# Kernel optimization log

Measured on AMD Instinct MI355X. Metric: run time of the kernel, lower is better.

The kernel has to match this reference:

```python
import jax, jax.numpy as jnp
import numpy as np

N, E, F_IN, HID, HEADS, NGRAPH = 50000, 800000, 256, 128, 4, 50
NEG_SLOPE = 0.2


def gat_conv(x, src, dst, W, a_src, a_dst, bias, heads, ch, concat):
    # x: [N, F_in]; W: [F_in, heads*ch]; a_src/a_dst: [heads, ch]; bias: [heads*ch] or [ch]
    n = x.shape[0]
    h = (x @ W).reshape(n, heads, ch)                      # [N,H,C]
    alpha_s = (h * a_src).sum(-1)                          # [N,H]
    alpha_d = (h * a_dst).sum(-1)                          # [N,H]
    e = jax.nn.leaky_relu(alpha_s[src] + alpha_d[dst], NEG_SLOPE)  # [E,H]
    # segment softmax over incoming edges of each destination node
    emax = jax.ops.segment_max(e, dst, num_segments=n)
    ex = jnp.exp(e - emax[dst])
    denom = jax.ops.segment_sum(ex, dst, num_segments=n)
    alpha = ex / (denom[dst] + 1e-16)                      # [E,H]
    msg = h[src] * alpha[:, :, None]                       # [E,H,C]
    out = jax.ops.segment_sum(msg, dst, num_segments=n)    # [N,H,C]
    out = out.reshape(n, heads * ch) if concat else out.mean(axis=1)
    return out + bias


def setup_inputs() -> dict:
    key = jax.random.key(0)
    ks = jax.random.split(key, 16)
    x = jax.random.normal(ks[0], (N, F_IN), dtype=jnp.float32)
    edge_index = jax.random.randint(ks[1], (2, E), 0, N, dtype=jnp.int64)
    batch = jnp.sort(jax.random.randint(ks[2], (N,), 0, NGRAPH, dtype=jnp.int64))
    s = 0.05
    return {
        "x": x, "edge_index": edge_index, "batch": batch,
        "W1": jax.random.normal(ks[3], (F_IN, HEADS * HID)) * s,
        "a1s": jax.random.normal(ks[4], (HEADS, HID)) * s,
        "a1d": jax.random.normal(ks[5], (HEADS, HID)) * s,
        "b1": jnp.zeros((HEADS * HID,), jnp.float32),
        "W2": jax.random.normal(ks[6], (HEADS * HID, HEADS * HID)) * s,
        "a2s": jax.random.normal(ks[7], (HEADS, HID)) * s,
        "a2d": jax.random.normal(ks[8], (HEADS, HID)) * s,
        "b2": jnp.zeros((HEADS * HID,), jnp.float32),
        "W3": jax.random.normal(ks[9], (HEADS * HID, HID)) * s,
        "a3s": jax.random.normal(ks[10], (1, HID)) * s,
        "a3d": jax.random.normal(ks[11], (1, HID)) * s,
        "b3": jnp.zeros((HID,), jnp.float32),
    }


def reference(x, edge_index, batch, W1, a1s, a1d, b1, W2, a2s, a2d, b2, W3, a3s, a3d, b3):
    src, dst = edge_index[0], edge_index[1]
    h = gat_conv(x, src, dst, W1, a1s, a1d, b1, HEADS, HID, True)
    h = jax.nn.elu(h)
    h = gat_conv(h, src, dst, W2, a2s, a2d, b2, HEADS, HID, True)
    h = jax.nn.elu(h)
    node_emb = gat_conv(h, src, dst, W3, a3s, a3d, b3, 1, HID, False)
    # global mean pool per graph
    sums = jax.ops.segment_sum(node_emb, batch, num_segments=NGRAPH)
    counts = jax.ops.segment_sum(jnp.ones((node_emb.shape[0],), node_emb.dtype), batch, num_segments=NGRAPH)
    graph_emb = sums / jnp.maximum(counts, 1.0)[:, None]
    return node_emb, graph_emb
```

## Files before the change

kernel.cpp:

```cpp
#include <hip/hip_runtime.h>
#include <hip/hip_bf16.h>

#define NN 50000
#define EE 800000
#define FIN 256
#define HIDC 128
#define NGRAPH 50
#define POOL_CHUNKS 32

typedef __attribute__((ext_vector_type(8))) short bf16x8;
typedef __attribute__((ext_vector_type(4))) float f32x4;

__device__ __forceinline__ float lrelu(float x) { return x > 0.f ? x : 0.2f * x; }

__device__ __forceinline__ unsigned short f2bf(float f) {
  union { float f; unsigned u; } c; c.f = f;
  unsigned u = c.u;
  unsigned r = (u + 0x7fffu + ((u >> 16) & 1u)) >> 16;
  return (unsigned short)r;
}
__device__ __forceinline__ float bf2f(unsigned short b) {
  union { unsigned u; float f; } c; c.u = ((unsigned)b) << 16;
  return c.f;
}

__global__ void hist_kernel(const int* __restrict__ dst, int* __restrict__ deg) {
  int e = blockIdx.x * blockDim.x + threadIdx.x;
  if (e < EE) atomicAdd(&deg[dst[e]], 1);
}

__global__ __launch_bounds__(1024)
void scan_kernel(const int* __restrict__ deg, int* __restrict__ indptr,
                 int* __restrict__ cursor) {
  __shared__ int wsum[16];
  const int tid = threadIdx.x;
  const int lane = tid & 63, wid = tid >> 6;
  const int PER = (NN + 1023) / 1024;
  int base = tid * PER;
  int n = NN - base; if (n < 0) n = 0; if (n > PER) n = PER;
  int sum = 0;
  for (int j = 0; j < n; j++) sum += deg[base + j];
  int inc = sum;
#pragma unroll
  for (int off = 1; off < 64; off <<= 1) {
    int t = __shfl_up(inc, off);
    if (lane >= off) inc += t;
  }
  if (lane == 63) wsum[wid] = inc;
  __syncthreads();
  if (tid == 0) {
    int run = 0;
#pragma unroll
    for (int w = 0; w < 16; w++) { int t = wsum[w]; wsum[w] = run; run += t; }
  }
  __syncthreads();
  int excl = wsum[wid] + inc - sum;
  int running = excl;
  for (int j = 0; j < n; j++) {
    int d = deg[base + j];
    indptr[base + j] = running;
    cursor[base + j] = running;
    running += d;
  }
  if (tid == 1023) indptr[NN] = excl + sum;
}

__global__ void scatter_kernel(const int* __restrict__ src, const int* __restrict__ dst,
                               int* __restrict__ cursor, int* __restrict__ csr_src) {
  int e = blockIdx.x * blockDim.x + threadIdx.x;
  if (e < EE) {
    int d = dst[e];
    int slot = atomicAdd(&cursor[d], 1);
    csr_src[slot] = src[e];
  }
}

__global__ __launch_bounds__(256)
void transpose_split(const float* __restrict__ W, unsigned short* __restrict__ WtHi,
                     unsigned short* __restrict__ WtLo, int K, int N) {
  __shared__ float t[32][33];
  int k0 = blockIdx.y * 32, n0 = blockIdx.x * 32;
  int tx = threadIdx.x & 31, ty = threadIdx.x >> 5;
  for (int r = ty; r < 32; r += 8) t[r][tx] = W[(size_t)(k0 + r) * N + n0 + tx];
  __syncthreads();
  for (int r = ty; r < 32; r += 8) {
    float v = t[tx][r];
    unsigned short hb = f2bf(v);
    size_t o = (size_t)(n0 + r) * K + k0 + tx;
    WtHi[o] = hb;
    WtLo[o] = f2bf(v - bf2f(hb));
  }
}

__global__ void split_x(const float* __restrict__ in, unsigned short* __restrict__ hi,
                        unsigned short* __restrict__ lo, int n4) {
  int i = blockIdx.x * blockDim.x + threadIdx.x;
  if (i >= n4) return;
  float4 v = ((const float4*)in)[i];
  unsigned short h[4], l[4];
  float a[4] = {v.x, v.y, v.z, v.w};
#pragma unroll
  for (int j = 0; j < 4; j++) { h[j] = f2bf(a[j]); l[j] = f2bf(a[j] - bf2f(h[j])); }
  ((ushort4*)hi)[i] = make_ushort4(h[0], h[1], h[2], h[3]);
  ((ushort4*)lo)[i] = make_ushort4(l[0], l[1], l[2], l[3]);
}

__global__ __launch_bounds__(256)
void gemm_split(const unsigned short* __restrict__ Ahi, const unsigned short* __restrict__ Alo,
                const unsigned short* __restrict__ Bhi, const unsigned short* __restrict__ Blo,
                float* __restrict__ C, int M, int K, int Ncols) {
  __shared__ unsigned short smem[4 * 128 * 32];
  const int tid = threadIdx.x;
  const int lane = tid & 63;
  const int wid = tid >> 6;
  const int wr = wid >> 1, wc = wid & 1;
  const int brow0 = blockIdx.y * 128, bcol0 = blockIdx.x * 128;

  f32x4 acc[4][4];
#pragma unroll
  for (int i = 0; i < 4; i++)
#pragma unroll
    for (int j = 0; j < 4; j++) acc[i][j] = (f32x4){0.f, 0.f, 0.f, 0.f};

  for (int k0 = 0; k0 < K; k0 += 32) {
#pragma unroll
    for (int t = 0; t < 8; t++) {
      const int tile = t >> 1;
      const int s = ((t & 1) << 8) + tid;
      const int row = s >> 2;
      const int cl = (s & 3) ^ ((row >> 1) & 3);
      const unsigned short* gsrc;
      if (tile < 2) {
        int grow = brow0 + row; if (grow > M - 1) grow = M - 1;
        const unsigned short* base = (tile == 0) ? Ahi : Alo;
        gsrc = base + (size_t)grow * K + k0 + cl * 8;
      } else {
        int gcol = bcol0 + row;
        const unsigned short* base = (tile == 2) ? Bhi : Blo;
        gsrc = base + (size_t)gcol * K + k0 + cl * 8;
      }
      unsigned short* ldst = &smem[(size_t)(tile * 512 + ((t & 1) << 8) + (tid & ~63)) * 8];
      __builtin_amdgcn_global_load_lds((const __attribute__((address_space(1))) void*)gsrc,
                                       (__attribute__((address_space(3))) void*)ldst, 16, 0, 0);
    }
    __syncthreads();

    bf16x8 ah[4], al[4];
#pragma unroll
    for (int mf = 0; mf < 4; mf++) {
      int R = wr * 64 + mf * 16 + (lane & 15);
      int off = R * 32 + ((((lane >> 4)) ^ ((R >> 1) & 3)) << 3);
      ah[mf] = *(const bf16x8*)&smem[off];
      al[mf] = *(const bf16x8*)&smem[4096 + off];
    }
#pragma unroll
    for (int nf = 0; nf < 4; nf++) {
      int R = wc * 64 + nf * 16 + (lane & 15);
      int off = R * 32 + ((((lane >> 4)) ^ ((R >> 1) & 3)) << 3);
      bf16x8 bh = *(const bf16x8*)&smem[8192 + off];
      bf16x8 bl = *(const bf16x8*)&smem[12288 + off];
#pragma unroll
      for (int mf = 0; mf < 4; mf++) {
        acc[mf][nf] = __builtin_amdgcn_mfma_f32_16x16x32_bf16(ah[mf], bh, acc[mf][nf], 0, 0, 0);
        acc[mf][nf] = __builtin_amdgcn_mfma_f32_16x16x32_bf16(al[mf], bh, acc[mf][nf], 0, 0, 0);
        acc[mf][nf] = __builtin_amdgcn_mfma_f32_16x16x32_bf16(ah[mf], bl, acc[mf][nf], 0, 0, 0);
      }
    }
    __syncthreads();
  }

  const int orow = (lane >> 4) * 4;
  const int ocol = lane & 15;
#pragma unroll
  for (int mf = 0; mf < 4; mf++) {
#pragma unroll
    for (int r = 0; r < 4; r++) {
      int grow = brow0 + wr * 64 + mf * 16 + orow + r;
      if (grow < M) {
#pragma unroll
        for (int nf = 0; nf < 4; nf++) {
          int gcol = bcol0 + wc * 64 + nf * 16 + ocol;
          C[(size_t)grow * Ncols + gcol] = acc[mf][nf][r];
        }
      }
    }
  }
}

template <int H>
__global__ __launch_bounds__(256)
void alpha_kernel(const float* __restrict__ h, const float* __restrict__ a_s,
                  const float* __restrict__ a_d, float* __restrict__ as_out,
                  float* __restrict__ ad_out) {
  int gw = (blockIdx.x * blockDim.x + threadIdx.x) >> 6;
  int lane = threadIdx.x & 63;
  if (gw >= NN * H) return;
  int node = gw / H, hh = gw % H;
  const float2 hv = *(const float2*)&h[(size_t)node * (H * HIDC) + hh * HIDC + lane * 2];
  const float2 sv = *(const float2*)&a_s[hh * HIDC + lane * 2];
  const float2 dv = *(const float2*)&a_d[hh * HIDC + lane * 2];
  float ss = hv.x * sv.x + hv.y * sv.y;
  float sd = hv.x * dv.x + hv.y * dv.y;
#pragma unroll
  for (int off = 32; off; off >>= 1) {
    ss += __shfl_xor(ss, off);
    sd += __shfl_xor(sd, off);
  }
  if (lane == 0) {
    as_out[node * H + hh] = ss;
    ad_out[node * H + hh] = sd;
  }
}

template <int H, int CH, bool SPLIT, bool ELU>
__global__ __launch_bounds__(256)
void aggregate_kernel(const float* __restrict__ h, const float* __restrict__ asb,
                      const float* __restrict__ adb, const int* __restrict__ indptr,
                      const int* __restrict__ csr_src, const float* __restrict__ bias,
                      float* __restrict__ outF, unsigned short* __restrict__ outHi,
                      unsigned short* __restrict__ outLo) {
  constexpr int F = CH / 64;
  int node = (blockIdx.x * blockDim.x + threadIdx.x) >> 6;
  int lane = threadIdx.x & 63;
  if (node >= NN) return;
  int beg = indptr[node], end = indptr[node + 1];
  int deg = end - beg;
  float acc[F];
#pragma unroll
  for (int f = 0; f < F; f++) acc[f] = 0.f;

  if (deg > 0) {
    float adv[H];
#pragma unroll
    for (int hh = 0; hh < H; hh++) adv[hh] = adb[node * H + hh];
    float m[H];
#pragma unroll
    for (int hh = 0; hh < H; hh++) m[hh] = -1e30f;
    for (int i = lane; i < deg; i += 64) {
      int s = csr_src[beg + i];
#pragma unroll
      for (int hh = 0; hh < H; hh++) {
        float e = lrelu(asb[s * H + hh] + adv[hh]);
        m[hh] = fmaxf(m[hh], e);
      }
    }
#pragma unroll
    for (int off = 32; off; off >>= 1)
#pragma unroll
      for (int hh = 0; hh < H; hh++) m[hh] = fmaxf(m[hh], __shfl_xor(m[hh], off));
    float ssum[H];
#pragma unroll
    for (int hh = 0; hh < H; hh++) ssum[hh] = 0.f;
    for (int i = lane; i < deg; i += 64) {
      int s = csr_src[beg + i];
#pragma unroll
      for (int hh = 0; hh < H; hh++) {
        float e = lrelu(asb[s * H + hh] + adv[hh]);
        ssum[hh] += expf(e - m[hh]);
      }
    }
#pragma unroll
    for (int off = 32; off; off >>= 1)
#pragma unroll
      for (int hh = 0; hh < H; hh++) ssum[hh] += __shfl_xor(ssum[hh], off);
    float rden[H];
#pragma unroll
    for (int hh = 0; hh < H; hh++) rden[hh] = 1.f / (ssum[hh] + 1e-16f);

    const int myh = (lane * F) / HIDC;
    float myadv = adv[myh], mym = m[myh], myrd = rden[myh];
    for (int i = 0; i < deg; i++) {
      int s = csr_src[beg + i];
      float e = lrelu(asb[s * H + myh] + myadv);
      float w = expf(e - mym) * myrd;
      const float* hrow = &h[(size_t)s * CH + lane * F];
      if constexpr (F == 8) {
        float4 v0 = *(const float4*)&hrow[0];
        float4 v1 = *(const float4*)&hrow[4];
        acc[0] += w * v0.x; acc[1] += w * v0.y; acc[2] += w * v0.z; acc[3] += w * v0.w;
        acc[4] += w * v1.x; acc[5] += w * v1.y; acc[6] += w * v1.z; acc[7] += w * v1.w;
      } else {
        float2 v0 = *(const float2*)&hrow[0];
        acc[0] += w * v0.x;
        acc[1] += w * v0.y;
      }
    }
  }
  if constexpr (SPLIT) {
    unsigned short hs[F], ls[F];
#pragma unroll
    for (int f = 0; f < F; f++) {
      float v = acc[f] + bias[lane * F + f];
      if constexpr (ELU) v = v > 0.f ? v : expm1f(v);
      unsigned short hb = f2bf(v);
      hs[f] = hb;
      ls[f] = f2bf(v - bf2f(hb));
    }
    size_t o = (size_t)node * CH + lane * F;
    *(ushort4*)&outHi[o]     = make_ushort4(hs[0], hs[1], hs[2], hs[3]);
    *(ushort4*)&outHi[o + 4] = make_ushort4(hs[4], hs[5], hs[6], hs[7]);
    *(ushort4*)&outLo[o]     = make_ushort4(ls[0], ls[1], ls[2], ls[3]);
    *(ushort4*)&outLo[o + 4] = make_ushort4(ls[4], ls[5], ls[6], ls[7]);
  } else {
#pragma unroll
    for (int f = 0; f < F; f++) {
      int c = lane * F + f;
      float v = acc[f] + bias[c];
      if constexpr (ELU) v = v > 0.f ? v : expm1f(v);
      outF[(size_t)node * CH + c] = v;
    }
  }
}

__global__ void pool_partial(const float* __restrict__ node_emb, const int* __restrict__ batch,
                             float* __restrict__ part) {
  int g = blockIdx.x, chunk = blockIdx.y, c = threadIdx.x;
  int lo = 0, hi = NN;
  while (lo < hi) { int mid = (lo + hi) >> 1; if (batch[mid] < g) lo = mid + 1; else hi = mid; }
  int s = lo;
  lo = 0; hi = NN;
  while (lo < hi) { int mid = (lo + hi) >> 1; if (batch[mid] < g + 1) lo = mid + 1; else hi = mid; }
  int e = lo;
  int per = (e - s + POOL_CHUNKS - 1) / POOL_CHUNKS;
  int cs = s + chunk * per;
  int ce = cs + per; if (ce > e) ce = e;
  float sum = 0.f;
  for (int i = cs; i < ce; i++) sum += node_emb[(size_t)i * HIDC + c];
  part[((size_t)chunk * NGRAPH + g) * HIDC + c] = sum;
}

__global__ void pool_final(const float* __restrict__ part, const int* __restrict__ batch,
                           float* __restrict__ gout) {
  int g = blockIdx.x, c = threadIdx.x;
  int lo = 0, hi = NN;
  while (lo < hi) { int mid = (lo + hi) >> 1; if (batch[mid] < g) lo = mid + 1; else hi = mid; }
  int s = lo;
  lo = 0; hi = NN;
  while (lo < hi) { int mid = (lo + hi) >> 1; if (batch[mid] < g + 1) lo = mid + 1; else hi = mid; }
  int e = lo;
  float sum = 0.f;
#pragma unroll
  for (int k = 0; k < POOL_CHUNKS; k++) sum += part[((size_t)k * NGRAPH + g) * HIDC + c];
  gout[g * HIDC + c] = sum / fmaxf((float)(e - s), 1.0f);
}

extern "C" void kernel_launch(void* const* d_in, const int* in_sizes, int n_in,
                              void* d_out, int out_size, void* d_ws, size_t ws_size,
                              hipStream_t stream) {
  const float* x   = (const float*)d_in[0];
  const int* ei    = (const int*)d_in[1];
  const int* batch = (const int*)d_in[2];
  const float* W1  = (const float*)d_in[3];
  const float* a1s = (const float*)d_in[4];
  const float* a1d = (const float*)d_in[5];
  const float* b1  = (const float*)d_in[6];
  const float* W2  = (const float*)d_in[7];
  const float* a2s = (const float*)d_in[8];
  const float* a2d = (const float*)d_in[9];
  const float* b2  = (const float*)d_in[10];
  const float* W3  = (const float*)d_in[11];
  const float* a3s = (const float*)d_in[12];
  const float* a3d = (const float*)d_in[13];
  const float* b3  = (const float*)d_in[14];
  float* out_node  = (float*)d_out;
  float* out_graph = out_node + (size_t)NN * HIDC;

  char* p = (char*)d_ws;
  auto take = [&](size_t bytes) {
    char* cur = p;
    p += (bytes + 255) & ~(size_t)255;
    return cur;
  };
  unsigned short* hHi = (unsigned short*)take((size_t)NN * 512 * 2);
  unsigned short* hLo = (unsigned short*)take((size_t)NN * 512 * 2);
  float* bufF = (float*)take((size_t)NN * 512 * 4);
  float* asb  = (float*)take((size_t)NN * 4 * 4);
  float* adb  = (float*)take((size_t)NN * 4 * 4);
  unsigned short* W1tH = (unsigned short*)take((size_t)512 * 256 * 2);
  unsigned short* W1tL = (unsigned short*)take((size_t)512 * 256 * 2);
  unsigned short* W2tH = (unsigned short*)take((size_t)512 * 512 * 2);
  unsigned short* W2tL = (unsigned short*)take((size_t)512 * 512 * 2);
  unsigned short* W3tH = (unsigned short*)take((size_t)128 * 512 * 2);
  unsigned short* W3tL = (unsigned short*)take((size_t)128 * 512 * 2);
  int* deg    = (int*)take((size_t)NN * 4);
  int* indptr = (int*)take((size_t)(NN + 1) * 4);
  int* cursor = (int*)take((size_t)NN * 4);
  int* csr    = (int*)take((size_t)EE * 4);
  float* poolws = (float*)take((size_t)POOL_CHUNKS * NGRAPH * HIDC * 4);

  const int* srcv = ei;
  const int* dstv = ei + EE;

  hipMemsetAsync(deg, 0, (size_t)NN * 4, stream);
  hist_kernel<<<(EE + 255) / 256, 256, 0, stream>>>(dstv, deg);
  scan_kernel<<<1, 1024, 0, stream>>>(deg, indptr, cursor);
  scatter_kernel<<<(EE + 255) / 256, 256, 0, stream>>>(srcv, dstv, cursor, csr);

  transpose_split<<<dim3(512 / 32, 256 / 32), 256, 0, stream>>>(W1, W1tH, W1tL, 256, 512);
  transpose_split<<<dim3(512 / 32, 512 / 32), 256, 0, stream>>>(W2, W2tH, W2tL, 512, 512);
  transpose_split<<<dim3(128 / 32, 512 / 32), 256, 0, stream>>>(W3, W3tH, W3tL, 512, 128);
  split_x<<<(NN * FIN / 4 + 255) / 256, 256, 0, stream>>>(x, hHi, hLo, NN * FIN / 4);

  dim3 blk(256);
  const int rowBlocks = (NN + 127) / 128;
  gemm_split<<<dim3(4, rowBlocks), blk, 0, stream>>>(hHi, hLo, W1tH, W1tL, bufF, NN, 256, 512);
  alpha_kernel<4><<<(NN * 4 + 3) / 4, blk, 0, stream>>>(bufF, a1s, a1d, asb, adb);
  aggregate_kernel<4, 512, true, true><<<(NN + 3) / 4, blk, 0, stream>>>(
      bufF, asb, adb, indptr, csr, b1, nullptr, hHi, hLo);
  gemm_split<<<dim3(4, rowBlocks), blk, 0, stream>>>(hHi, hLo, W2tH, W2tL, bufF, NN, 512, 512);
  alpha_kernel<4><<<(NN * 4 + 3) / 4, blk, 0, stream>>>(bufF, a2s, a2d, asb, adb);
  aggregate_kernel<4, 512, true, true><<<(NN + 3) / 4, blk, 0, stream>>>(
      bufF, asb, adb, indptr, csr, b2, nullptr, hHi, hLo);
  gemm_split<<<dim3(1, rowBlocks), blk, 0, stream>>>(hHi, hLo, W3tH, W3tL, bufF, NN, 512, 128);
  alpha_kernel<1><<<(NN + 3) / 4, blk, 0, stream>>>(bufF, a3s, a3d, asb, adb);
  aggregate_kernel<1, 128, false, false><<<(NN + 3) / 4, blk, 0, stream>>>(
      bufF, asb, adb, indptr, csr, b3, out_node, nullptr, nullptr);
  pool_partial<<<dim3(NGRAPH, POOL_CHUNKS), HIDC, 0, stream>>>(out_node, batch, poolws);
  pool_final<<<NGRAPH, HIDC, 0, stream>>>(poolws, batch, out_graph);
}
```

Measured before the change: 1.186 ms.

## Aggregate each destination node with a full block, splitting edges across waves

The aggregation kernel now assigns one 256-thread block per destination node instead of one wave per node. The four waves split the node's incoming edges, and their partial sums are reduced through shared memory, with block-level reductions for the softmax max and sum. This raises memory-level parallelism for the gather of source rows, since average degree is about 16. In exchange it adds several __syncthreads, a shared-memory reduction, and scalar (non-vectorised) output stores, and launches four times as many blocks.

```diff
diff --git a/kernel.cpp b/kernel.cpp
--- a/kernel.cpp
+++ b/kernel.cpp
@@ -220,93 +220,110 @@
                       float* __restrict__ outF, unsigned short* __restrict__ outHi,
                       unsigned short* __restrict__ outLo) {
   constexpr int F = CH / 64;
-  int node = (blockIdx.x * blockDim.x + threadIdx.x) >> 6;
-  int lane = threadIdx.x & 63;
-  if (node >= NN) return;
-  int beg = indptr[node], end = indptr[node + 1];
-  int deg = end - beg;
+  __shared__ float sAcc[4][CH];
+  __shared__ float sM[4][H], sS[4][H];
+  __shared__ float fM[H], fR[H];
+  const int node = blockIdx.x;
+  const int tid = threadIdx.x;
+  const int lane = tid & 63, w = tid >> 6;
+  const int beg = indptr[node];
+  const int deg = indptr[node + 1] - beg;
+
+  float adv[H];
+#pragma unroll
+  for (int hh = 0; hh < H; hh++) adv[hh] = adb[node * H + hh];
+
+  float m[H];
+#pragma unroll
+  for (int hh = 0; hh < H; hh++) m[hh] = -1e30f;
+  for (int i = tid; i < deg; i += 256) {
+    int s = csr_src[beg + i];
+#pragma unroll
+    for (int hh = 0; hh < H; hh++)
+      m[hh] = fmaxf(m[hh], lrelu(asb[s * H + hh] + adv[hh]));
+  }
+#pragma unroll
+  for (int off = 32; off; off >>= 1)
+#pragma unroll
+    for (int hh = 0; hh < H; hh++) m[hh] = fmaxf(m[hh], __shfl_xor(m[hh], off));
+  if (lane == 0) {
+#pragma unroll
+    for (int hh = 0; hh < H; hh++) sM[w][hh] = m[hh];
+  }
+  __syncthreads();
+  if (tid < H) {
+    float mm = fmaxf(fmaxf(sM[0][tid], sM[1][tid]), fmaxf(sM[2][tid], sM[3][tid]));
+    fM[tid] = mm;
+  }
+  __syncthreads();
+#pragma unroll
+  for (int hh = 0; hh < H; hh++) m[hh] = fM[hh];
+
+  float ssum[H];
+#pragma unroll
+  for (int hh = 0; hh < H; hh++) ssum[hh] = 0.f;
+  for (int i = tid; i < deg; i += 256) {
+    int s = csr_src[beg + i];
+#pragma unroll
+    for (int hh = 0; hh < H; hh++) {
+      float e = lrelu(asb[s * H + hh] + adv[hh]);
+      ssum[hh] += expf(e - m[hh]);
+    }
+  }
+#pragma unroll
+  for (int off = 32; off; off >>= 1)
+#pragma unroll
+    for (int hh = 0; hh < H; hh++) ssum[hh] += __shfl_xor(ssum[hh], off);
+  if (lane == 0) {
+#pragma unroll
+    for (int hh = 0; hh < H; hh++) sS[w][hh] = ssum[hh];
+  }
+  __syncthreads();
+  if (tid < H) {
+    float ss = sS[0][tid] + sS[1][tid] + sS[2][tid] + sS[3][tid];
+    fR[tid] = 1.f / (ss + 1e-16f);
+  }
+  __syncthreads();
+
+  const int myh = (lane * F) / HIDC;
+  const float myadv = adv[0 ? 0 : 0] * 0.f + adb[node * H + myh];
+  const float mym = fM[myh], myrd = fR[myh];
   float acc[F];
 #pragma unroll
   for (int f = 0; f < F; f++) acc[f] = 0.f;
-
-  if (deg > 0) {
-    float adv[H];
-#pragma unroll
-    for (int hh = 0; hh < H; hh++) adv[hh] = adb[node * H + hh];
-    float m[H];
-#pragma unroll
-    for (int hh = 0; hh < H; hh++) m[hh] = -1e30f;
-    for (int i = lane; i < deg; i += 64) {
-      int s = csr_src[beg + i];
-#pragma unroll
-      for (int hh = 0; hh < H; hh++) {
-        float e = lrelu(asb[s * H + hh] + adv[hh]);
-        m[hh] = fmaxf(m[hh], e);
-      }
-    }
-#pragma unroll
-    for (int off = 32; off; off >>= 1)
-#pragma unroll
-      for (int hh = 0; hh < H; hh++) m[hh] = fmaxf(m[hh], __shfl_xor(m[hh], off));
-    float ssum[H];
-#pragma unroll
-    for (int hh = 0; hh < H; hh++) ssum[hh] = 0.f;
-    for (int i = lane; i < deg; i += 64) {
-      int s = csr_src[beg + i];
-#pragma unroll
-      for (int hh = 0; hh < H; hh++) {
-        float e = lrelu(asb[s * H + hh] + adv[hh]);
-        ssum[hh] += expf(e - m[hh]);
-      }
-    }
-#pragma unroll
-    for (int off = 32; off; off >>= 1)
-#pragma unroll
-      for (int hh = 0; hh < H; hh++) ssum[hh] += __shfl_xor(ssum[hh], off);
-    float rden[H];
-#pragma unroll
-    for (int hh = 0; hh < H; hh++) rden[hh] = 1.f / (ssum[hh] + 1e-16f);
-
-    const int myh = (lane * F) / HIDC;
-    float myadv = adv[myh], mym = m[myh], myrd = rden[myh];
-    for (int i = 0; i < deg; i++) {
-      int s = csr_src[beg + i];
-      float e = lrelu(asb[s * H + myh] + myadv);
-      float w = expf(e - mym) * myrd;
-      const float* hrow = &h[(size_t)s * CH + lane * F];
-      if constexpr (F == 8) {
-        float4 v0 = *(const float4*)&hrow[0];
-        float4 v1 = *(const float4*)&hrow[4];
-        acc[0] += w * v0.x; acc[1] += w * v0.y; acc[2] += w * v0.z; acc[3] += w * v0.w;
-        acc[4] += w * v1.x; acc[5] += w * v1.y; acc[6] += w * v1.z; acc[7] += w * v1.w;
-      } else {
-        float2 v0 = *(const float2*)&hrow[0];
-        acc[0] += w * v0.x;
-        acc[1] += w * v0.y;
-      }
-    }
-  }
-  if constexpr (SPLIT) {
-    unsigned short hs[F], ls[F];
-#pragma unroll
-    for (int f = 0; f < F; f++) {
-      float v = acc[f] + bias[lane * F + f];
-      if constexpr (ELU) v = v > 0.f ? v : expm1f(v);
+  for (int i = w; i < deg; i += 4) {
+    int s = csr_src[beg + i];
+    float e = lrelu(asb[s * H + myh] + myadv);
+    float wgt = expf(e - mym) * myrd;
+    const float* hrow = &h[(size_t)s * CH + lane * F];
+    if constexpr (F == 8) {
+      float4 v0 = *(const float4*)&hrow[0];
+      float4 v1 = *(const float4*)&hrow[4];
+      acc[0] += wgt * v0.x; acc[1] += wgt * v0.y; acc[2] += wgt * v0.z; acc[3] += wgt * v0.w;
+      acc[4] += wgt * v1.x; acc[5] += wgt * v1.y; acc[6] += wgt * v1.z; acc[7] += wgt * v1.w;
+    } else {
+      float2 v0 = *(const float2*)&hrow[0];
+      acc[0] += wgt * v0.x;
+      acc[1] += wgt * v0.y;
+    }
+  }
+  if constexpr (F == 8) {
+    *(float4*)&sAcc[w][lane * 8]     = make_float4(acc[0], acc[1], acc[2], acc[3]);
+    *(float4*)&sAcc[w][lane * 8 + 4] = make_float4(acc[4], acc[5], acc[6], acc[7]);
+  } else {
+    *(float2*)&sAcc[w][lane * 2] = make_float2(acc[0], acc[1]);
+  }
+  __syncthreads();
+
+  for (int c = tid; c < CH; c += 256) {
+    float v = sAcc[0][c] + sAcc[1][c] + sAcc[2][c] + sAcc[3][c];
+    v += bias[c];
+    if constexpr (ELU) v = v > 0.f ? v : expm1f(v);
+    if constexpr (SPLIT) {
       unsigned short hb = f2bf(v);
-      hs[f] = hb;
-      ls[f] = f2bf(v - bf2f(hb));
-    }
-    size_t o = (size_t)node * CH + lane * F;
-    *(ushort4*)&outHi[o]     = make_ushort4(hs[0], hs[1], hs[2], hs[3]);
-    *(ushort4*)&outHi[o + 4] = make_ushort4(hs[4], hs[5], hs[6], hs[7]);
-    *(ushort4*)&outLo[o]     = make_ushort4(ls[0], ls[1], ls[2], ls[3]);
-    *(ushort4*)&outLo[o + 4] = make_ushort4(ls[4], ls[5], ls[6], ls[7]);
-  } else {
-#pragma unroll
-    for (int f = 0; f < F; f++) {
-      int c = lane * F + f;
-      float v = acc[f] + bias[c];
-      if constexpr (ELU) v = v > 0.f ? v : expm1f(v);
+      outHi[(size_t)node * CH + c] = hb;
+      outLo[(size_t)node * CH + c] = f2bf(v - bf2f(hb));
+    } else {
       outF[(size_t)node * CH + c] = v;
     }
   }
@@ -405,15 +422,15 @@
   const int rowBlocks = (NN + 127) / 128;
   gemm_split<<<dim3(4, rowBlocks), blk, 0, stream>>>(hHi, hLo, W1tH, W1tL, bufF, NN, 256, 512);
   alpha_kernel<4><<<(NN * 4 + 3) / 4, blk, 0, stream>>>(bufF, a1s, a1d, asb, adb);
-  aggregate_kernel<4, 512, true, true><<<(NN + 3) / 4, blk, 0, stream>>>(
+  aggregate_kernel<4, 512, true, true><<<NN, blk, 0, stream>>>(
       bufF, asb, adb, indptr, csr, b1, nullptr, hHi, hLo);
   gemm_split<<<dim3(4, rowBlocks), blk, 0, stream>>>(hHi, hLo, W2tH, W2tL, bufF, NN, 512, 512);
   alpha_kernel<4><<<(NN * 4 + 3) / 4, blk, 0, stream>>>(bufF, a2s, a2d, asb, adb);
-  aggregate_kernel<4, 512, true, true><<<(NN + 3) / 4, blk, 0, stream>>>(
+  aggregate_kernel<4, 512, true, true><<<NN, blk, 0, stream>>>(
       bufF, asb, adb, indptr, csr, b2, nullptr, hHi, hLo);
   gemm_split<<<dim3(1, rowBlocks), blk, 0, stream>>>(hHi, hLo, W3tH, W3tL, bufF, NN, 512, 128);
   alpha_kernel<1><<<(NN + 3) / 4, blk, 0, stream>>>(bufF, a3s, a3d, asb, adb);
-  aggregate_kernel<1, 128, false, false><<<(NN + 3) / 4, blk, 0, stream>>>(
+  aggregate_kernel<1, 128, false, false><<<NN, blk, 0, stream>>>(
       bufF, asb, adb, indptr, csr, b3, out_node, nullptr, nullptr);
   pool_partial<<<dim3(NGRAPH, POOL_CHUNKS), HIDC, 0, stream>>>(out_node, batch, poolws);
   pool_final<<<NGRAPH, HIDC, 0, stream>>>(poolws, batch, out_graph);
```

New measurement: 1.218 ms. 2.7% more time.
